# Kernel tuning notes

Measured on AMD Instinct MI355X. Metric: run time of the kernel, lower is better.

## Reference

```python
import jax, jax.numpy as jnp
import numpy as np

BS, CIN, H, W = 1, 128, 448, 96
CLASSES = (8, 8, 8)
PAD = (0, 4, 4)
DIV = 1  # c3_line_div
K2 = H * CLASSES[0]                 # 3584 CondMul experts for stage 2
K3 = H * CLASSES[0] * CLASSES[1]    # 28672 CondMul experts for stage 3
C1_DIMS = [(128, 32), (32, 32), (32, 8)]
C2_DIMS = [(128, 32), (32, 32), (32, 16)]
C3_DIMS = [(128, 32), (32, 32), (32, 16)]


def _cond_mul(x, inds, w, b):
    # per-row expert gather then small matmul: [N,i] x [N,i,o] -> [N,o]
    return jnp.einsum('ni,nio->no', x, w[inds]) + b[inds]


def setup_inputs() -> dict:
    key = jax.random.key(0)
    ks = jax.random.split(key, 19)
    d = {'x_in': jax.random.normal(ks[0], (BS, CIN, H, W), jnp.float32)}
    k = 1
    for tag, dims, nexp in (('1', C1_DIMS, H), ('2', C2_DIMS, K2), ('3', C3_DIMS, K3)):
        for i, (ci, co) in enumerate(dims):
            if tag == '1':
                d['w1_%d' % i] = jax.random.normal(ks[k], (H, co, ci), jnp.float32) * 0.1
            else:
                d['w%s_%d' % (tag, i)] = jax.random.normal(ks[k], (nexp, ci, co), jnp.float32) * 0.1
            d['b%s_%d' % (tag, i)] = jax.random.normal(ks[k + 1], (nexp, co), jnp.float32) * 0.1
            k += 2
    return d


def reference(x_in, w1_0, b1_0, w1_1, b1_1, w1_2, b1_2,
              w2_0, b2_0, w2_1, b2_1, w2_2, b2_2,
              w3_0, b3_0, w3_1, b3_1, w3_2, b3_2):
    bs, cin, h, w = x_in.shape
    c12 = CLASSES[0] * CLASSES[1]
    c123 = c12 * CLASSES[2]
    lrelu = jax.nn.leaky_relu  # slope 0.01, matches F.leaky_relu default
    hoff = jnp.arange(h, dtype=jnp.int32)[None, :, None]  # [1,H,1] line offsets

    # stage 1: grouped 1x1 conv (one group per image line)
    x = jnp.transpose(x_in, (0, 2, 1, 3))  # [bs,H,C,W]
    x = lrelu(jnp.einsum('hoi,bhiw->bhow', w1_0, x) + b1_0[None, :, :, None])
    x = lrelu(jnp.einsum('hoi,bhiw->bhow', w1_1, x) + b1_1[None, :, :, None])
    x = jnp.einsum('hoi,bhiw->bhow', w1_2, x) + b1_2[None, :, :, None]  # [bs,H,cls1,W]
    inds1 = jnp.argmax(x, axis=2).astype(jnp.int32)  # [bs,H,W]
    inds1_l = (inds1 + CLASSES[0] * hoff).reshape(-1)  # [N]

    x_l = jnp.transpose(x_in, (0, 2, 3, 1)).reshape(-1, cin)  # [N,C], N=bs*H*W

    # stage 2: CondMul cascade routed by inds1
    x = lrelu(_cond_mul(x_l, inds1_l, w2_0, b2_0))
    x = lrelu(_cond_mul(x, inds1_l, w2_1, b2_1))
    x = _cond_mul(x, inds1_l, w2_2, b2_2)
    inds2 = jnp.argmax(x, axis=-1).astype(jnp.int32).reshape(bs, h, w)
    inds12 = inds1 * CLASSES[1] + (inds2 - PAD[1])
    inds12_cl = jnp.clip(inds12, 0, c12 - 1)
    inds12_l = (inds12_cl + c12 * hoff).reshape(-1)
    inds12_s = (inds12_cl + c12 * (hoff // DIV)).reshape(-1)

    # stage 3: CondMul cascade routed by inds12
    x = lrelu(_cond_mul(x_l, inds12_s, w3_0, b3_0))
    x = lrelu(_cond_mul(x, inds12_s, w3_1, b3_1))
    x3 = _cond_mul(x, inds12_l, w3_2, b3_2)  # [N, cls3+2*pad3]
    inds3 = jnp.argmax(x3, axis=-1).astype(jnp.int32).reshape(bs, h, w)

    inds123 = jnp.clip(inds12 * CLASSES[2] + (inds3 - PAD[2]), 0, c123 - 1)
    return inds123.reshape(bs, 1, h, w)
```

## Files before the change

### kernel.cpp

```cpp
#include <hip/hip_runtime.h>

#define H_ 448
#define CIN_ 128
#define HW_ (448*96)
#define PPB 48

__device__ __forceinline__ float lrelu(float v){ return v > 0.0f ? v : 0.01f*v; }

__device__ __forceinline__ void decode_block(int d, int& h, int& wb){
    const int r = d & 15, q = d >> 4;
    h  = (r & 7) + (q << 3);
    wb = (r >> 3) * PPB;
}

template<int NC>
__device__ __forceinline__ void sort_by_class(const unsigned char* s_cls, short* s_perm,
                                              int* s_cnt, int* s_off, int t)
{
    if (t < NC){
        int c = 0;
        for (int p = 0; p < PPB; p++) if (s_cls[p] == (unsigned char)t) c++;
        s_cnt[t] = c;
    }
    __syncthreads();
    if (t == 0){
        int a = 0;
        for (int c = 0; c < NC; c++){ s_off[c] = a; a += s_cnt[c]; }
    }
    __syncthreads();
    if (t < NC){
        int o = s_off[t];
        for (int p = 0; p < PPB; p++) if (s_cls[p] == (unsigned char)t) s_perm[o++] = (short)p;
    }
    __syncthreads();
}

__global__ __launch_bounds__(384, 4)
void k1_stage1(const float* __restrict__ X,
               const float* __restrict__ w1_0, const float* __restrict__ b1_0,
               const float* __restrict__ w1_1, const float* __restrict__ b1_1,
               const float* __restrict__ w1_2, const float* __restrict__ b1_2,
               unsigned char* __restrict__ inds1)
{
    __shared__ float s_w0[4096];
    __shared__ float s_w1[1024];
    __shared__ float s_w2[256];
    __shared__ float s_A[PPB*33];
    __shared__ float s_B[PPB*33];

    int h, wb; decode_block(blockIdx.x, h, wb);
    const int t  = threadIdx.x;
    const int w  = t % PPB;
    const int s  = t / PPB;
    const int hw = h*96 + wb + w;

    const float* g0 = w1_0 + (size_t)h*4096;
    for (int j = t; j < 4096; j += 384) s_w0[j] = g0[j];
    const float* g1 = w1_1 + (size_t)h*1024;
    for (int j = t; j < 1024; j += 384) s_w1[j] = g1[j];
    const float* g2 = w1_2 + (size_t)h*256;
    for (int j = t; j < 256; j += 384) s_w2[j] = g2[j];
    __syncthreads();

    {
        float acc[4];
        const float* bp = b1_0 + h*32 + s*4;
        #pragma unroll
        for (int k=0;k<4;k++) acc[k] = bp[k];
        #pragma unroll 4
        for (int i4=0;i4<32;i4++){
            const float x0 = X[(size_t)(4*i4+0)*HW_ + hw];
            const float x1 = X[(size_t)(4*i4+1)*HW_ + hw];
            const float x2 = X[(size_t)(4*i4+2)*HW_ + hw];
            const float x3 = X[(size_t)(4*i4+3)*HW_ + hw];
            #pragma unroll
            for (int k=0;k<4;k++){
                const float4 q = *(const float4*)&s_w0[(s*4+k)*128 + 4*i4];
                acc[k] += x0*q.x; acc[k] += x1*q.y; acc[k] += x2*q.z; acc[k] += x3*q.w;
            }
        }
        #pragma unroll
        for (int k=0;k<4;k++) s_A[w*33 + s*4 + k] = lrelu(acc[k]);
    }
    __syncthreads();

    {
        float acc[4];
        const float* bp = b1_1 + h*32 + s*4;
        #pragma unroll
        for (int k=0;k<4;k++) acc[k] = bp[k];
        #pragma unroll
        for (int i4=0;i4<8;i4++){
            const float x0 = s_A[w*33 + 4*i4+0];
            const float x1 = s_A[w*33 + 4*i4+1];
            const float x2 = s_A[w*33 + 4*i4+2];
            const float x3 = s_A[w*33 + 4*i4+3];
            #pragma unroll
            for (int k=0;k<4;k++){
                const float4 q = *(const float4*)&s_w1[(s*4+k)*32 + 4*i4];
                acc[k] += x0*q.x; acc[k] += x1*q.y; acc[k] += x2*q.z; acc[k] += x3*q.w;
            }
        }
        #pragma unroll
        for (int k=0;k<4;k++) s_B[w*33 + s*4 + k] = lrelu(acc[k]);
    }
    __syncthreads();

    {
        float acc = b1_2[h*8 + s];
        #pragma unroll
        for (int i4=0;i4<8;i4++){
            const float4 q = *(const float4*)&s_w2[s*32 + 4*i4];
            acc += s_B[w*33 + 4*i4+0]*q.x;
            acc += s_B[w*33 + 4*i4+1]*q.y;
            acc += s_B[w*33 + 4*i4+2]*q.z;
            acc += s_B[w*33 + 4*i4+3]*q.w;
        }
        s_A[w*33 + s] = acc;
    }
    __syncthreads();

    if (s == 0){
        const float* sc = &s_A[w*33];
        float best = sc[0]; int bi = 0;
        #pragma unroll
        for (int k=1;k<8;k++){ const float v = sc[k]; if (v > best){ best = v; bi = k; } }
        inds1[hw] = (unsigned char)bi;
    }
}

__global__ __launch_bounds__(384, 4)
void k2_stage2(const float* __restrict__ X,
               const float* __restrict__ w0, const float* __restrict__ b0,
               const float* __restrict__ w1, const float* __restrict__ b1,
               const float* __restrict__ w2, const float* __restrict__ b2,
               const unsigned char* __restrict__ inds1,
               signed char* __restrict__ raw12, unsigned char* __restrict__ cls2)
{
    __shared__ float s_A[PPB*36];
    __shared__ float s_B[PPB*36];
    __shared__ unsigned char s_cls[PPB];
    __shared__ short s_perm[PPB];
    __shared__ int   s_cnt[8];
    __shared__ int   s_off[8];

    int h, wb; decode_block(blockIdx.x, h, wb);
    const int t = threadIdx.x;
    if (t < PPB) s_cls[t] = inds1[h*96 + wb + t];
    __syncthreads();
    sort_by_class<8>(s_cls, s_perm, s_cnt, s_off, t);

    const int p = t >> 3;
    const int j = t & 7;
    const int sp = s_perm[p];
    const int c  = s_cls[sp];
    const long e = (long)h*8 + c;
    const int hw = h*96 + wb + sp;
    const float* W0 = w0 + e*4096 + j*4;
    const float* W1 = w1 + e*1024 + j*4;
    const float* W2 = w2 + e*512  + j*2;

    float4 acc = *(const float4*)&b0[e*32 + j*4];
    #pragma unroll 8
    for (int i=0;i<128;i++){
        const float xv = X[(size_t)i*HW_ + hw];
        const float4 q = *(const float4*)&W0[i*32];
        acc.x += xv*q.x; acc.y += xv*q.y; acc.z += xv*q.z; acc.w += xv*q.w;
    }
    *(float4*)&s_A[p*36 + j*4] = make_float4(lrelu(acc.x),lrelu(acc.y),lrelu(acc.z),lrelu(acc.w));
    __syncthreads();

    float4 ac2 = *(const float4*)&b1[e*32 + j*4];
    #pragma unroll 8
    for (int i=0;i<32;i++){
        const float xv = s_A[p*36 + i];
        const float4 q = *(const float4*)&W1[i*32];
        ac2.x += xv*q.x; ac2.y += xv*q.y; ac2.z += xv*q.z; ac2.w += xv*q.w;
    }
    *(float4*)&s_B[p*36 + j*4] = make_float4(lrelu(ac2.x),lrelu(ac2.y),lrelu(ac2.z),lrelu(ac2.w));
    __syncthreads();

    float2 sc = *(const float2*)&b2[e*16 + j*2];
    #pragma unroll 8
    for (int i=0;i<32;i++){
        const float xv = s_B[p*36 + i];
        const float2 r = *(const float2*)&W2[i*16];
        sc.x += xv*r.x; sc.y += xv*r.y;
    }
    float best = sc.x; int bi = j*2;
    if (sc.y > best){ best = sc.y; bi = j*2+1; }
    #pragma unroll
    for (int off=1; off<8; off<<=1){
        const float ob = __shfl_xor(best, off, 64);
        const int  obi = __shfl_xor(bi,  off, 64);
        if (ob > best || (ob == best && obi < bi)){ best = ob; bi = obi; }
    }
    if (j == 0){
        const int raw = c*8 + bi - 4;
        raw12[hw] = (signed char)raw;
        cls2[hw]  = (unsigned char)(raw < 0 ? 0 : (raw > 63 ? 63 : raw));
    }
}

__global__ __launch_bounds__(384, 4)
void k3_stage3(const float* __restrict__ X,
               const float* __restrict__ w0, const float* __restrict__ b0,
               const float* __restrict__ w1, const float* __restrict__ b1,
               const float* __restrict__ w2, const float* __restrict__ b2,
               const unsigned char* __restrict__ cls2,
               const signed char* __restrict__ raw12,
               int* __restrict__ out)
{
    __shared__ float s_A[PPB*36];
    __shared__ float s_B[PPB*36];
    __shared__ unsigned char s_cls[PPB];
    __shared__ short s_perm[PPB];
    __shared__ int   s_cnt[64];
    __shared__ int   s_off[64];

    int h, wb; decode_block(blockIdx.x, h, wb);
    const int t = threadIdx.x;
    if (t < PPB) s_cls[t] = cls2[h*96 + wb + t];
    __syncthreads();
    sort_by_class<64>(s_cls, s_perm, s_cnt, s_off, t);

    const int p = t >> 3;
    const int j = t & 7;
    const int sp = s_perm[p];
    const int c  = s_cls[sp];
    const long e = (long)h*64 + c;
    const int hw = h*96 + wb + sp;
    const float* W0 = w0 + e*4096 + j*4;
    const float* W1 = w1 + e*1024 + j*4;
    const float* W2 = w2 + e*512  + j*2;

    float4 acc = *(const float4*)&b0[e*32 + j*4];
    #pragma unroll 8
    for (int i=0;i<128;i++){
        const float xv = X[(size_t)i*HW_ + hw];
        const float4 q = *(const float4*)&W0[i*32];
        acc.x += xv*q.x; acc.y += xv*q.y; acc.z += xv*q.z; acc.w += xv*q.w;
    }
    *(float4*)&s_A[p*36 + j*4] = make_float4(lrelu(acc.x),lrelu(acc.y),lrelu(acc.z),lrelu(acc.w));
    __syncthreads();

    float4 ac2 = *(const float4*)&b1[e*32 + j*4];
    #pragma unroll 8
    for (int i=0;i<32;i++){
        const float xv = s_A[p*36 + i];
        const float4 q = *(const float4*)&W1[i*32];
        ac2.x += xv*q.x; ac2.y += xv*q.y; ac2.z += xv*q.z; ac2.w += xv*q.w;
    }
    *(float4*)&s_B[p*36 + j*4] = make_float4(lrelu(ac2.x),lrelu(ac2.y),lrelu(ac2.z),lrelu(ac2.w));
    __syncthreads();

    float2 sc = *(const float2*)&b2[e*16 + j*2];
    #pragma unroll 8
    for (int i=0;i<32;i++){
        const float xv = s_B[p*36 + i];
        const float2 r = *(const float2*)&W2[i*16];
        sc.x += xv*r.x; sc.y += xv*r.y;
    }
    float best = sc.x; int bi = j*2;
    if (sc.y > best){ best = sc.y; bi = j*2+1; }
    #pragma unroll
    for (int off=1; off<8; off<<=1){
        const float ob = __shfl_xor(best, off, 64);
        const int  obi = __shfl_xor(bi,  off, 64);
        if (ob > best || (ob == best && obi < bi)){ best = ob; bi = obi; }
    }
    if (j == 0){
        int v = (int)raw12[hw]*8 + bi - 4;
        v = v < 0 ? 0 : (v > 511 ? 511 : v);
        out[hw] = v;
    }
}

extern "C" void kernel_launch(void* const* d_in, const int* in_sizes, int n_in,
                              void* d_out, int out_size, void* d_ws, size_t ws_size,
                              hipStream_t stream) {
    const float* X    = (const float*)d_in[0];
    const float* w1_0 = (const float*)d_in[1];
    const float* b1_0 = (const float*)d_in[2];
    const float* w1_1 = (const float*)d_in[3];
    const float* b1_1 = (const float*)d_in[4];
    const float* w1_2 = (const float*)d_in[5];
    const float* b1_2 = (const float*)d_in[6];
    const float* w2_0 = (const float*)d_in[7];
    const float* b2_0 = (const float*)d_in[8];
    const float* w2_1 = (const float*)d_in[9];
    const float* b2_1 = (const float*)d_in[10];
    const float* w2_2 = (const float*)d_in[11];
    const float* b2_2 = (const float*)d_in[12];
    const float* w3_0 = (const float*)d_in[13];
    const float* b3_0 = (const float*)d_in[14];
    const float* w3_1 = (const float*)d_in[15];
    const float* b3_1 = (const float*)d_in[16];
    const float* w3_2 = (const float*)d_in[17];
    const float* b3_2 = (const float*)d_in[18];
    int* out = (int*)d_out;

    unsigned char* inds1 = (unsigned char*)d_ws;
    unsigned char* cls2  = inds1 + HW_;
    signed char*   raw12 = (signed char*)(cls2 + HW_);

    k1_stage1<<<H_*2, 384, 0, stream>>>(X, w1_0, b1_0, w1_1, b1_1, w1_2, b1_2, inds1);
    k2_stage2<<<H_*2, 384, 0, stream>>>(X, w2_0, b2_0, w2_1, b2_1, w2_2, b2_2, inds1, raw12, cls2);
    k3_stage3<<<H_*2, 384, 0, stream>>>(X, w3_0, b3_0, w3_1, b3_1, w3_2, b3_2, cls2, raw12, out);
}
```

Measured before the change: 155.4 us.

## Process same-class pixel pairs per thread group to reuse expert weight loads

The two CondMul stage kernels are merged into one templated kernel. In it, each 8-thread group handles two pixels routed to the same expert, so every weight float4 loaded from global memory is used twice. A serial per-block pass on thread 0 builds the list of pairs. The block-wide barriers between layers are dropped because each group reads back only the shared-memory rows it wrote itself. This roughly halves weight traffic when classes repeat within a block, but leaves about half the groups idle and adds serial pair-building work on one thread.

```diff
diff --git a/kernel.cpp b/kernel.cpp
--- a/kernel.cpp
+++ b/kernel.cpp
@@ -31,6 +31,21 @@
     if (t < NC){
         int o = s_off[t];
         for (int p = 0; p < PPB; p++) if (s_cls[p] == (unsigned char)t) s_perm[o++] = (short)p;
+    }
+    __syncthreads();
+}
+
+template<int NC>
+__device__ __forceinline__ void build_pairs(const int* s_cnt, const int* s_off,
+                                            int* s_chunk, int* s_nch, int t)
+{
+    if (t == 0){
+        int n = 0;
+        for (int c = 0; c < NC; c++){
+            const int cnt = s_cnt[c];
+            for (int b = 0; b < cnt; b += 2) s_chunk[n++] = (c << 16) | (s_off[c] + b);
+        }
+        *s_nch = n;
     }
     __syncthreads();
 }
@@ -129,150 +144,130 @@
     }
 }
 
+template<int NC, bool S3>
 __global__ __launch_bounds__(384, 4)
-void k2_stage2(const float* __restrict__ X,
-               const float* __restrict__ w0, const float* __restrict__ b0,
-               const float* __restrict__ w1, const float* __restrict__ b1,
-               const float* __restrict__ w2, const float* __restrict__ b2,
-               const unsigned char* __restrict__ inds1,
-               signed char* __restrict__ raw12, unsigned char* __restrict__ cls2)
+void condmul_pair(const float* __restrict__ X,
+                  const float* __restrict__ w0, const float* __restrict__ b0,
+                  const float* __restrict__ w1, const float* __restrict__ b1,
+                  const float* __restrict__ w2, const float* __restrict__ b2,
+                  const unsigned char* __restrict__ route,
+                  signed char* __restrict__ raw12,
+                  unsigned char* __restrict__ cls2,
+                  int* __restrict__ out)
 {
     __shared__ float s_A[PPB*36];
     __shared__ float s_B[PPB*36];
     __shared__ unsigned char s_cls[PPB];
     __shared__ short s_perm[PPB];
-    __shared__ int   s_cnt[8];
-    __shared__ int   s_off[8];
+    __shared__ int   s_cnt[NC];
+    __shared__ int   s_off[NC];
+    __shared__ int   s_chunk[PPB];
+    __shared__ int   s_nch;
 
     int h, wb; decode_block(blockIdx.x, h, wb);
     const int t = threadIdx.x;
-    if (t < PPB) s_cls[t] = inds1[h*96 + wb + t];
-    __syncthreads();
-    sort_by_class<8>(s_cls, s_perm, s_cnt, s_off, t);
-
-    const int p = t >> 3;
+    if (t < PPB) s_cls[t] = route[h*96 + wb + t];
+    __syncthreads();
+    sort_by_class<NC>(s_cls, s_perm, s_cnt, s_off, t);
+    build_pairs<NC>(s_cnt, s_off, s_chunk, &s_nch, t);
+
+    const int g = t >> 3;
     const int j = t & 7;
-    const int sp = s_perm[p];
-    const int c  = s_cls[sp];
-    const long e = (long)h*8 + c;
-    const int hw = h*96 + wb + sp;
+    if (g >= s_nch) return;
+
+    const int info = s_chunk[g];
+    const int c    = info >> 16;
+    const int base = info & 0xffff;
+    const bool has2 = (base + 1) < (s_off[c] + s_cnt[c]);
+    const int sp0 = s_perm[base];
+    const int sp1 = has2 ? s_perm[base + 1] : sp0;
+    const long e = (long)h*NC + c;
+    const int hw0 = h*96 + wb + sp0;
+    const int hw1 = h*96 + wb + sp1;
     const float* W0 = w0 + e*4096 + j*4;
     const float* W1 = w1 + e*1024 + j*4;
     const float* W2 = w2 + e*512  + j*2;
 
-    float4 acc = *(const float4*)&b0[e*32 + j*4];
+    float4 a0, a1;
+    a0 = a1 = *(const float4*)&b0[e*32 + j*4];
     #pragma unroll 8
     for (int i=0;i<128;i++){
-        const float xv = X[(size_t)i*HW_ + hw];
         const float4 q = *(const float4*)&W0[i*32];
-        acc.x += xv*q.x; acc.y += xv*q.y; acc.z += xv*q.z; acc.w += xv*q.w;
-    }
-    *(float4*)&s_A[p*36 + j*4] = make_float4(lrelu(acc.x),lrelu(acc.y),lrelu(acc.z),lrelu(acc.w));
-    __syncthreads();
-
-    float4 ac2 = *(const float4*)&b1[e*32 + j*4];
+        const float x0 = X[(size_t)i*HW_ + hw0];
+        const float x1 = X[(size_t)i*HW_ + hw1];
+        a0.x += x0*q.x; a0.y += x0*q.y; a0.z += x0*q.z; a0.w += x0*q.w;
+        a1.x += x1*q.x; a1.y += x1*q.y; a1.z += x1*q.z; a1.w += x1*q.w;
+    }
+    *(float4*)&s_A[sp0*36 + j*4] = make_float4(lrelu(a0.x),lrelu(a0.y),lrelu(a0.z),lrelu(a0.w));
+    if (has2)
+        *(float4*)&s_A[sp1*36 + j*4] = make_float4(lrelu(a1.x),lrelu(a1.y),lrelu(a1.z),lrelu(a1.w));
+
+    float4 c0, c1;
+    c0 = c1 = *(const float4*)&b1[e*32 + j*4];
     #pragma unroll 8
     for (int i=0;i<32;i++){
-        const float xv = s_A[p*36 + i];
         const float4 q = *(const float4*)&W1[i*32];
-        ac2.x += xv*q.x; ac2.y += xv*q.y; ac2.z += xv*q.z; ac2.w += xv*q.w;
-    }
-    *(float4*)&s_B[p*36 + j*4] = make_float4(lrelu(ac2.x),lrelu(ac2.y),lrelu(ac2.z),lrelu(ac2.w));
-    __syncthreads();
-
-    float2 sc = *(const float2*)&b2[e*16 + j*2];
+        const float x0 = s_A[sp0*36 + i];
+        const float x1 = s_A[sp1*36 + i];
+        c0.x += x0*q.x; c0.y += x0*q.y; c0.z += x0*q.z; c0.w += x0*q.w;
+        c1.x += x1*q.x; c1.y += x1*q.y; c1.z += x1*q.z; c1.w += x1*q.w;
+    }
+    *(float4*)&s_B[sp0*36 + j*4] = make_float4(lrelu(c0.x),lrelu(c0.y),lrelu(c0.z),lrelu(c0.w));
+    if (has2)
+        *(float4*)&s_B[sp1*36 + j*4] = make_float4(lrelu(c1.x),lrelu(c1.y),lrelu(c1.z),lrelu(c1.w));
+
+    float2 d0, d1;
+    d0 = d1 = *(const float2*)&b2[e*16 + j*2];
     #pragma unroll 8
     for (int i=0;i<32;i++){
-        const float xv = s_B[p*36 + i];
         const float2 r = *(const float2*)&W2[i*16];
-        sc.x += xv*r.x; sc.y += xv*r.y;
-    }
-    float best = sc.x; int bi = j*2;
-    if (sc.y > best){ best = sc.y; bi = j*2+1; }
-    #pragma unroll
-    for (int off=1; off<8; off<<=1){
-        const float ob = __shfl_xor(best, off, 64);
-        const int  obi = __shfl_xor(bi,  off, 64);
-        if (ob > best || (ob == best && obi < bi)){ best = ob; bi = obi; }
-    }
-    if (j == 0){
-        const int raw = c*8 + bi - 4;
-        raw12[hw] = (signed char)raw;
-        cls2[hw]  = (unsigned char)(raw < 0 ? 0 : (raw > 63 ? 63 : raw));
-    }
-}
-
-__global__ __launch_bounds__(384, 4)
-void k3_stage3(const float* __restrict__ X,
-               const float* __restrict__ w0, const float* __restrict__ b0,
-               const float* __restrict__ w1, const float* __restrict__ b1,
-               const float* __restrict__ w2, const float* __restrict__ b2,
-               const unsigned char* __restrict__ cls2,
-               const signed char* __restrict__ raw12,
-               int* __restrict__ out)
-{
-    __shared__ float s_A[PPB*36];
-    __shared__ float s_B[PPB*36];
-    __shared__ unsigned char s_cls[PPB];
-    __shared__ short s_perm[PPB];
-    __shared__ int   s_cnt[64];
-    __shared__ int   s_off[64];
-
-    int h, wb; decode_block(blockIdx.x, h, wb);
-    const int t = threadIdx.x;
-    if (t < PPB) s_cls[t] = cls2[h*96 + wb + t];
-    __syncthreads();
-    sort_by_class<64>(s_cls, s_perm, s_cnt, s_off, t);
-
-    const int p = t >> 3;
-    const int j = t & 7;
-    const int sp = s_perm[p];
-    const int c  = s_cls[sp];
-    const long e = (long)h*64 + c;
-    const int hw = h*96 + wb + sp;
-    const float* W0 = w0 + e*4096 + j*4;
-    const float* W1 = w1 + e*1024 + j*4;
-    const float* W2 = w2 + e*512  + j*2;
-
-    float4 acc = *(const float4*)&b0[e*32 + j*4];
-    #pragma unroll 8
-    for (int i=0;i<128;i++){
-        const float xv = X[(size_t)i*HW_ + hw];
-        const float4 q = *(const float4*)&W0[i*32];
-        acc.x += xv*q.x; acc.y += xv*q.y; acc.z += xv*q.z; acc.w += xv*q.w;
-    }
-    *(float4*)&s_A[p*36 + j*4] = make_float4(lrelu(acc.x),lrelu(acc.y),lrelu(acc.z),lrelu(acc.w));
-    __syncthreads();
-
-    float4 ac2 = *(const float4*)&b1[e*32 + j*4];
-    #pragma unroll 8
-    for (int i=0;i<32;i++){
-        const float xv = s_A[p*36 + i];
-        const float4 q = *(const float4*)&W1[i*32];
-        ac2.x += xv*q.x; ac2.y += xv*q.y; ac2.z += xv*q.z; ac2.w += xv*q.w;
-    }
-    *(float4*)&s_B[p*36 + j*4] = make_float4(lrelu(ac2.x),lrelu(ac2.y),lrelu(ac2.z),lrelu(ac2.w));
-    __syncthreads();
-
-    float2 sc = *(const float2*)&b2[e*16 + j*2];
-    #pragma unroll 8
-    for (int i=0;i<32;i++){
-        const float xv = s_B[p*36 + i];
-        const float2 r = *(const float2*)&W2[i*16];
-        sc.x += xv*r.x; sc.y += xv*r.y;
-    }
-    float best = sc.x; int bi = j*2;
-    if (sc.y > best){ best = sc.y; bi = j*2+1; }
-    #pragma unroll
-    for (int off=1; off<8; off<<=1){
-        const float ob = __shfl_xor(best, off, 64);
-        const int  obi = __shfl_xor(bi,  off, 64);
-        if (ob > best || (ob == best && obi < bi)){ best = ob; bi = obi; }
-    }
-    if (j == 0){
-        int v = (int)raw12[hw]*8 + bi - 4;
-        v = v < 0 ? 0 : (v > 511 ? 511 : v);
-        out[hw] = v;
+        const float x0 = s_B[sp0*36 + i];
+        const float x1 = s_B[sp1*36 + i];
+        d0.x += x0*r.x; d0.y += x0*r.y;
+        d1.x += x1*r.x; d1.y += x1*r.y;
+    }
+
+    {
+        float best = d0.x; int bi = j*2;
+        if (d0.y > best){ best = d0.y; bi = j*2+1; }
+        #pragma unroll
+        for (int off=1; off<8; off<<=1){
+            const float ob = __shfl_xor(best, off, 64);
+            const int  obi = __shfl_xor(bi,  off, 64);
+            if (ob > best || (ob == best && obi < bi)){ best = ob; bi = obi; }
+        }
+        if (j == 0){
+            if (S3){
+                int v = (int)raw12[hw0]*8 + bi - 4;
+                v = v < 0 ? 0 : (v > 511 ? 511 : v);
+                out[hw0] = v;
+            } else {
+                const int raw = c*8 + bi - 4;
+                raw12[hw0] = (signed char)raw;
+                cls2[hw0]  = (unsigned char)(raw < 0 ? 0 : (raw > 63 ? 63 : raw));
+            }
+        }
+    }
+    if (has2){
+        float best = d1.x; int bi = j*2;
+        if (d1.y > best){ best = d1.y; bi = j*2+1; }
+        #pragma unroll
+        for (int off=1; off<8; off<<=1){
+            const float ob = __shfl_xor(best, off, 64);
+            const int  obi = __shfl_xor(bi,  off, 64);
+            if (ob > best || (ob == best && obi < bi)){ best = ob; bi = obi; }
+        }
+        if (j == 0){
+            if (S3){
+                int v = (int)raw12[hw1]*8 + bi - 4;
+                v = v < 0 ? 0 : (v > 511 ? 511 : v);
+                out[hw1] = v;
+            } else {
+                const int raw = c*8 + bi - 4;
+                raw12[hw1] = (signed char)raw;
+                cls2[hw1]  = (unsigned char)(raw < 0 ? 0 : (raw > 63 ? 63 : raw));
+            }
+        }
     }
 }
 
@@ -305,6 +300,8 @@
     signed char*   raw12 = (signed char*)(cls2 + HW_);
 
     k1_stage1<<<H_*2, 384, 0, stream>>>(X, w1_0, b1_0, w1_1, b1_1, w1_2, b1_2, inds1);
-    k2_stage2<<<H_*2, 384, 0, stream>>>(X, w2_0, b2_0, w2_1, b2_1, w2_2, b2_2, inds1, raw12, cls2);
-    k3_stage3<<<H_*2, 384, 0, stream>>>(X, w3_0, b3_0, w3_1, b3_1, w3_2, b3_2, cls2, raw12, out);
-}
+    condmul_pair<8,  false><<<H_*2, 384, 0, stream>>>(X, w2_0, b2_0, w2_1, b2_1, w2_2, b2_2,
+                                                      inds1, raw12, cls2, out);
+    condmul_pair<64, true ><<<H_*2, 384, 0, stream>>>(X, w3_0, b3_0, w3_1, b3_1, w3_2, b3_2,
+                                                      cls2, raw12, cls2, out);
+}
```

After: 195.9 us. 1.26x slower.
